# Kernel tuning notes

Hardware: AMD Instinct MI355X
Metric: run time of the kernel (lower is better)

The kernel has to match this reference:

```python
import jax, jax.numpy as jnp
import numpy as np

N, M, H, R, F = 50000, 64, 128, 4, 7   # nodes, latent, hidden, rounds, node features
E = 800_000                             # directed edges
B, NMAX = 32, 512                       # dense-batch graphs, padded nodes per graph


def setup_inputs() -> dict:
    key = jax.random.key(0)
    ks = jax.random.split(key, 10)
    glorot = lambda k, shape, fan_in: (jax.random.normal(k, shape, jnp.float32)
                                       / np.float32(np.sqrt(fan_in)))
    return {
        "z": jax.random.normal(ks[0], (N, M), jnp.float32),
        "edge_index": jax.random.randint(ks[1], (2, E), 0, N, dtype=jnp.int32),
        "z_dense": jax.random.normal(ks[2], (B, NMAX, M), jnp.float32),
        "bias": jnp.zeros((1,), jnp.float32),
        "W_in": glorot(ks[3], (M, H), M), "b_in": jnp.zeros((H,), jnp.float32),
        "W_msg": glorot(ks[4], (R, H, H), H), "b_msg": jnp.zeros((R, H), jnp.float32),
        "W_upd": glorot(ks[5], (R, H, H), H), "b_upd": jnp.zeros((R, H), jnp.float32),
        "W_out": glorot(ks[6], (H, F), H), "b_out": jnp.zeros((F,), jnp.float32),
    }


def reference(z, edge_index, z_dense, bias, W_in, b_in, W_msg, b_msg,
              W_upd, b_upd, W_out, b_out):
    # decode_edges: (B, n_max, M) -> (B, n_max, n_max) inner-product logits + bias
    edge_logits = jnp.einsum("bnm,bkm->bnk", z_dense, z_dense) + bias[0]

    # decode_nodes: gather -> MLP -> scatter message passing
    src, dst = edge_index[0], edge_index[1]
    num_nodes = z.shape[0]
    state = jax.nn.relu(z @ W_in + b_in)                      # (N, H)
    for r in range(W_msg.shape[0]):                           # R small, fixed
        message = jax.nn.relu(state @ W_msg[r] + b_msg[r])    # (N, H)
        # aggregated[v] = sum_{(u->v) in E} message[u]
        aggregated = jax.ops.segment_sum(message[src], dst, num_segments=num_nodes)
        state = state + jax.nn.relu(aggregated @ W_upd[r] + b_upd[r])
    node_logits = state @ W_out + b_out                       # (N, F)

    return edge_logits, node_logits
```

## Files before the change

kernel.cpp:

```cpp
#include <hip/hip_runtime.h>
#include <cstdint>

#define NN  50000
#define MD  64
#define HD  128
#define RR  4
#define FD  7
#define EE  800000
#define BG  32
#define NMX 512

#define NH   196
#define NBL  196
#define BE   4096
#define NS   (NH * NBL)
#define NSB  ((NS + 255) / 256)

typedef __attribute__((ext_vector_type(8))) short bf16x8;
typedef __attribute__((ext_vector_type(4))) float f32x4;

__device__ __forceinline__ unsigned short f2bf(float f) {
    unsigned u = __builtin_bit_cast(unsigned, f);
    u = (u + 0x7fffu + ((u >> 16) & 1u)) >> 16;
    return (unsigned short)u;
}
__device__ __forceinline__ float bflo(unsigned u) { return __builtin_bit_cast(float, u << 16); }
__device__ __forceinline__ float bfhi(unsigned u) { return __builtin_bit_cast(float, u & 0xffff0000u); }

__device__ __forceinline__ bf16x8 pack8(float4 a, float4 b) {
    bf16x8 r;
    r[0]=(short)f2bf(a.x); r[1]=(short)f2bf(a.y); r[2]=(short)f2bf(a.z); r[3]=(short)f2bf(a.w);
    r[4]=(short)f2bf(b.x); r[5]=(short)f2bf(b.y); r[6]=(short)f2bf(b.z); r[7]=(short)f2bf(b.w);
    return r;
}

__global__ __launch_bounds__(256) void edge_kernel(const unsigned short* __restrict__ zdb,
                                                   const float* __restrict__ bias,
                                                   float* __restrict__ out) {
    __shared__ float cstage[64][68];
    const int b  = blockIdx.z;
    const int tn = blockIdx.y * 64;
    const int tk = blockIdx.x * 64;
    const unsigned short* zb = zdb + (size_t)b * NMX * MD;
    const int tid = threadIdx.x, wave = tid >> 6, lane = tid & 63;
    const int l15 = lane & 15, k8 = (lane >> 4) * 8;

    const unsigned short* ap = zb + (size_t)(tn + wave * 16 + l15) * MD + k8;
    bf16x8 af0 = *(const bf16x8*)ap;
    bf16x8 af1 = *(const bf16x8*)(ap + 32);

    f32x4 acc[4];
    #pragma unroll
    for (int ct = 0; ct < 4; ct++) acc[ct] = (f32x4){0.f, 0.f, 0.f, 0.f};
    const unsigned short* bp = zb + (size_t)(tk + l15) * MD + k8;
    #pragma unroll
    for (int ct = 0; ct < 4; ct++) {
        bf16x8 b0 = *(const bf16x8*)(bp + (size_t)ct * 16 * MD);
        bf16x8 b1 = *(const bf16x8*)(bp + (size_t)ct * 16 * MD + 32);
        acc[ct] = __builtin_amdgcn_mfma_f32_16x16x32_bf16(af0, b0, acc[ct], 0, 0, 0);
        acc[ct] = __builtin_amdgcn_mfma_f32_16x16x32_bf16(af1, b1, acc[ct], 0, 0, 0);
    }
    #pragma unroll
    for (int ct = 0; ct < 4; ct++)
        #pragma unroll
        for (int i = 0; i < 4; i++)
            cstage[wave * 16 + (lane >> 4) * 4 + i][ct * 16 + l15] = acc[ct][i];
    __syncthreads();
    const float bi = bias[0];
    #pragma unroll
    for (int it = 0; it < 4; it++) {
        int f = tid + it * 256;
        int row = f >> 4, c4 = (f & 15) * 4;
        float4 v = *(const float4*)&cstage[row][c4];
        v.x += bi; v.y += bi; v.z += bi; v.w += bi;
        *(float4*)(out + ((size_t)b * NMX + tn + row) * NMX + tk + c4) = v;
    }
}

__global__ __launch_bounds__(256) void cvt_kernel(const float* __restrict__ src,
                                                  unsigned short* __restrict__ dst,
                                                  int n4) {
    int i = blockIdx.x * 256 + threadIdx.x;
    if (i >= n4) return;
    float4 v = *(const float4*)(src + (size_t)i * 4);
    ushort4 o = {f2bf(v.x), f2bf(v.y), f2bf(v.z), f2bf(v.w)};
    *(ushort4*)(dst + (size_t)i * 4) = o;
}

__global__ __launch_bounds__(256) void tcvt_kernel(const float* __restrict__ src,
                                                   unsigned short* __restrict__ dst,
                                                   int K, int H) {
    int r = blockIdx.y;
    int i = blockIdx.x * 256 + threadIdx.x;
    if (i >= K * H) return;
    int k = i / H, h = i % H;
    float v = src[(size_t)r * K * H + i];
    dst[(size_t)r * K * H + (size_t)h * K + k] = f2bf(v);
}

template <int K1, int MODE>
__global__ __launch_bounds__(256) void fused_kernel(
    const unsigned short* __restrict__ in,
    const unsigned short* __restrict__ Wt1,
    const float* __restrict__ b1,
    float* __restrict__ state,
    const unsigned short* __restrict__ Wt2,
    const float* __restrict__ b2,
    unsigned short* __restrict__ msgb,
    const float* __restrict__ Wout,
    const float* __restrict__ bout,
    float* __restrict__ node_out,
    int nrows)
{
    constexpr int KC1 = K1 / 32;
    __shared__ float cstage[64][132];
    __shared__ float sWout[MODE == 2 ? HD * FD : 1];
    const int tid = threadIdx.x, wave = tid >> 6, lane = tid & 63;
    const int l15 = lane & 15, k8 = (lane >> 4) * 8;
    const int rbase = blockIdx.x * 64;

    if constexpr (MODE == 2)
        for (int i = tid; i < HD * FD; i += 256) sWout[i] = Wout[i];

    int rclamp = min(rbase + wave * 16 + l15, nrows - 1);
    bf16x8 af[KC1];
    #pragma unroll
    for (int c = 0; c < KC1; c++)
        af[c] = *(const bf16x8*)(in + (size_t)rclamp * K1 + (size_t)c * 32 + k8);
    f32x4 acc[8];
    #pragma unroll
    for (int ct = 0; ct < 8; ct++) acc[ct] = (f32x4){0.f, 0.f, 0.f, 0.f};
    const unsigned short* bp = Wt1 + (size_t)l15 * K1 + k8;
    #pragma unroll
    for (int ct = 0; ct < 8; ct++)
        #pragma unroll
        for (int c = 0; c < KC1; c++) {
            bf16x8 bf = *(const bf16x8*)(bp + (size_t)ct * 16 * K1 + c * 32);
            acc[ct] = __builtin_amdgcn_mfma_f32_16x16x32_bf16(af[c], bf, acc[ct], 0, 0, 0);
        }
    #pragma unroll
    for (int ct = 0; ct < 8; ct++)
        #pragma unroll
        for (int i = 0; i < 4; i++)
            cstage[wave * 16 + (lane >> 4) * 4 + i][ct * 16 + l15] = acc[ct][i];
    __syncthreads();

    #pragma unroll
    for (int it = 0; it < 8; it++) {
        int f = tid + it * 256;
        int row = f >> 5, c4 = (f & 31) * 4;
        int grow = rbase + row;
        if (grow < nrows) {
            float4 v = *(const float4*)&cstage[row][c4];
            float4 bb = *(const float4*)(b1 + c4);
            v.x = fmaxf(v.x + bb.x, 0.f);
            v.y = fmaxf(v.y + bb.y, 0.f);
            v.z = fmaxf(v.z + bb.z, 0.f);
            v.w = fmaxf(v.w + bb.w, 0.f);
            if constexpr (MODE >= 1) {
                float4 so = *(const float4*)(state + (size_t)grow * HD + c4);
                v.x += so.x; v.y += so.y; v.z += so.z; v.w += so.w;
            }
            if constexpr (MODE <= 1)
                *(float4*)(state + (size_t)grow * HD + c4) = v;
            *(float4*)&cstage[row][c4] = v;
        }
    }
    __syncthreads();

    if constexpr (MODE <= 1) {
        bf16x8 af2[4];
        #pragma unroll
        for (int c = 0; c < 4; c++) {
            float4 u0 = *(const float4*)&cstage[wave * 16 + l15][c * 32 + k8];
            float4 u1 = *(const float4*)&cstage[wave * 16 + l15][c * 32 + k8 + 4];
            af2[c] = pack8(u0, u1);
        }
        f32x4 acc2[8];
        #pragma unroll
        for (int ct = 0; ct < 8; ct++) acc2[ct] = (f32x4){0.f, 0.f, 0.f, 0.f};
        const unsigned short* bp2 = Wt2 + (size_t)l15 * HD + k8;
        #pragma unroll
        for (int ct = 0; ct < 8; ct++)
            #pragma unroll
            for (int c = 0; c < 4; c++) {
                bf16x8 bf = *(const bf16x8*)(bp2 + (size_t)ct * 16 * HD + c * 32);
                acc2[ct] = __builtin_amdgcn_mfma_f32_16x16x32_bf16(af2[c], bf, acc2[ct], 0, 0, 0);
            }
        __syncthreads();
        #pragma unroll
        for (int ct = 0; ct < 8; ct++)
            #pragma unroll
            for (int i = 0; i < 4; i++)
                cstage[wave * 16 + (lane >> 4) * 4 + i][ct * 16 + l15] = acc2[ct][i];
        __syncthreads();
        #pragma unroll
        for (int it = 0; it < 8; it++) {
            int f = tid + it * 256;
            int row = f >> 5, c4 = (f & 31) * 4;
            int grow = rbase + row;
            if (grow < nrows) {
                float4 v = *(const float4*)&cstage[row][c4];
                float4 bb = *(const float4*)(b2 + c4);
                v.x = fmaxf(v.x + bb.x, 0.f);
                v.y = fmaxf(v.y + bb.y, 0.f);
                v.z = fmaxf(v.z + bb.z, 0.f);
                v.w = fmaxf(v.w + bb.w, 0.f);
                ushort4 o = {f2bf(v.x), f2bf(v.y), f2bf(v.z), f2bf(v.w)};
                *(ushort4*)(msgb + (size_t)grow * HD + c4) = o;
            }
        }
    } else {
        for (int i = tid; i < 64 * FD; i += 256) {
            int row = i / FD, ff = i - row * FD;
            int grow = rbase + row;
            if (grow < nrows) {
                float a = bout[ff];
                #pragma unroll 8
                for (int k = 0; k < HD; k++)
                    a += cstage[row][k] * sWout[k * FD + ff];
                node_out[(size_t)grow * FD + ff] = a;
            }
        }
    }
}

__global__ __launch_bounds__(256) void p1c_kernel(const int* __restrict__ dst,
                                                  int* __restrict__ bh) {
    __shared__ int h[NH];
    const int b = blockIdx.x;
    for (int i = threadIdx.x; i < NH; i += 256) h[i] = 0;
    __syncthreads();
    const int e0 = b * BE;
    for (int i = threadIdx.x; i < BE; i += 256) {
        int e = e0 + i;
        if (e < EE) atomicAdd(&h[dst[e] >> 8], 1);
    }
    __syncthreads();
    for (int i = threadIdx.x; i < NH; i += 256) bh[i * NBL + b] = h[i];
}

__global__ __launch_bounds__(256) void scan1_kernel(const int* __restrict__ in,
                                                    int* __restrict__ incl,
                                                    int* __restrict__ bsum, int n) {
    __shared__ int s[256];
    int i = blockIdx.x * 256 + threadIdx.x;
    int t = threadIdx.x;
    s[t] = (i < n) ? in[i] : 0;
    __syncthreads();
    #pragma unroll
    for (int off = 1; off < 256; off <<= 1) {
        int x = (t >= off) ? s[t - off] : 0;
        __syncthreads();
        s[t] += x;
        __syncthreads();
    }
    if (i < n) incl[i] = s[t];
    if (t == 255) bsum[blockIdx.x] = s[255];
}

__global__ __launch_bounds__(256) void scan2_kernel(int* __restrict__ bsum, int nb) {
    __shared__ int s[256];
    int t = threadIdx.x;
    int orig = (t < nb) ? bsum[t] : 0;
    s[t] = orig;
    __syncthreads();
    #pragma unroll
    for (int off = 1; off < 256; off <<= 1) {
        int x = (t >= off) ? s[t - off] : 0;
        __syncthreads();
        s[t] += x;
        __syncthreads();
    }
    if (t < nb) bsum[t] = s[t] - orig;
}

__global__ __launch_bounds__(256) void scanex_kernel(const int* __restrict__ in,
                                                     const int* __restrict__ incl,
                                                     const int* __restrict__ bsum,
                                                     int* __restrict__ ex, int n) {
    int i = blockIdx.x * 256 + threadIdx.x;
    if (i < n) ex[i] = incl[i] - in[i] + bsum[blockIdx.x];
}

__global__ __launch_bounds__(256) void p1s_kernel(const int* __restrict__ src,
                                                  const int* __restrict__ dst,
                                                  const int* __restrict__ ex,
                                                  int2* __restrict__ sorted) {
    __shared__ int cur[NH];
    const int b = blockIdx.x;
    for (int i = threadIdx.x; i < NH; i += 256) cur[i] = ex[i * NBL + b];
    __syncthreads();
    const int e0 = b * BE;
    for (int i = threadIdx.x; i < BE; i += 256) {
        int e = e0 + i;
        if (e < EE) {
            int d = dst[e];
            int pos = atomicAdd(&cur[d >> 8], 1);
            sorted[pos] = make_int2(d, src[e]);
        }
    }
}

__global__ __launch_bounds__(256) void p2_kernel(const int2* __restrict__ sorted,
                                                 const int* __restrict__ ex,
                                                 int* __restrict__ row_ptr,
                                                 int* __restrict__ colsrc) {
    __shared__ int hist[256];
    __shared__ int scanb[256];
    __shared__ int cur[256];
    const int h = blockIdx.x;
    const int t = threadIdx.x;
    const int base = ex[h * NBL];
    const int endp = (h == NH - 1) ? EE : ex[(h + 1) * NBL];
    const int cnt  = endp - base;
    hist[t] = 0;
    __syncthreads();
    for (int i = t; i < cnt; i += 256)
        atomicAdd(&hist[sorted[base + i].x & 255], 1);
    __syncthreads();
    scanb[t] = hist[t];
    __syncthreads();
    #pragma unroll
    for (int off = 1; off < 256; off <<= 1) {
        int x = (t >= off) ? scanb[t - off] : 0;
        __syncthreads();
        scanb[t] += x;
        __syncthreads();
    }
    int excl = scanb[t] - hist[t];
    cur[t] = excl;
    int v = h * 256 + t;
    if (v < NN) row_ptr[v] = base + excl;
    if (h == NH - 1 && t == 0) row_ptr[NN] = EE;
    __syncthreads();
    for (int i = t; i < cnt; i += 256) {
        int2 pr = sorted[base + i];
        int pos = base + atomicAdd(&cur[pr.x & 255], 1);
        colsrc[pos] = pr.y;
    }
}

__global__ __launch_bounds__(256) void gather_kernel(const int* __restrict__ rp,
                                                     const int* __restrict__ colsrc,
                                                     const uint4* __restrict__ msg4,
                                                     uint4* __restrict__ agg4) {
    int v = blockIdx.x * 4 + (threadIdx.x >> 6);
    if (v >= NN) return;
    const int lane = threadIdx.x & 63;
    const int e = lane >> 4, q = lane & 15;
    const int beg = rp[v], end = rp[v + 1];
    float a[8];
    #pragma unroll
    for (int i = 0; i < 8; i++) a[i] = 0.f;

    int j = beg;
    for (; j + 7 < end; j += 8) {
        int c0 = colsrc[j + e];
        int c1 = colsrc[j + 4 + e];
        uint4 u = msg4[(size_t)c0 * 16 + q];
        uint4 w = msg4[(size_t)c1 * 16 + q];
        a[0] += bflo(u.x); a[1] += bfhi(u.x);
        a[2] += bflo(u.y); a[3] += bfhi(u.y);
        a[4] += bflo(u.z); a[5] += bfhi(u.z);
        a[6] += bflo(u.w); a[7] += bfhi(u.w);
        a[0] += bflo(w.x); a[1] += bfhi(w.x);
        a[2] += bflo(w.y); a[3] += bfhi(w.y);
        a[4] += bflo(w.z); a[5] += bfhi(w.z);
        a[6] += bflo(w.w); a[7] += bfhi(w.w);
    }
    for (; j < end; j += 4) {
        if (j + e < end) {
            uint4 u = msg4[(size_t)colsrc[j + e] * 16 + q];
            a[0] += bflo(u.x); a[1] += bfhi(u.x);
            a[2] += bflo(u.y); a[3] += bfhi(u.y);
            a[4] += bflo(u.z); a[5] += bfhi(u.z);
            a[6] += bflo(u.w); a[7] += bfhi(u.w);
        }
    }
    #pragma unroll
    for (int i = 0; i < 8; i++) {
        a[i] += __shfl_xor(a[i], 16);
        a[i] += __shfl_xor(a[i], 32);
    }
    if (lane < 16) {
        uint4 o;
        o.x = (unsigned)f2bf(a[0]) | ((unsigned)f2bf(a[1]) << 16);
        o.y = (unsigned)f2bf(a[2]) | ((unsigned)f2bf(a[3]) << 16);
        o.z = (unsigned)f2bf(a[4]) | ((unsigned)f2bf(a[5]) << 16);
        o.w = (unsigned)f2bf(a[6]) | ((unsigned)f2bf(a[7]) << 16);
        agg4[(size_t)v * 16 + q] = o;
    }
}

extern "C" void kernel_launch(void* const* d_in, const int* in_sizes, int n_in,
                              void* d_out, int out_size, void* d_ws, size_t ws_size,
                              hipStream_t stream) {
    const float* z          = (const float*)d_in[0];
    const int*   edge_index = (const int*)  d_in[1];
    const float* z_dense    = (const float*)d_in[2];
    const float* bias       = (const float*)d_in[3];
    const float* W_in       = (const float*)d_in[4];
    const float* b_in       = (const float*)d_in[5];
    const float* W_msg      = (const float*)d_in[6];
    const float* b_msg      = (const float*)d_in[7];
    const float* W_upd      = (const float*)d_in[8];
    const float* b_upd      = (const float*)d_in[9];
    const float* W_out      = (const float*)d_in[10];
    const float* b_out      = (const float*)d_in[11];

    float* out      = (float*)d_out;
    float* edge_out = out;
    float* node_out = out + (size_t)BG * NMX * NMX;

    char* p = (char*)d_ws;
    float* state = (float*)p;                     p += (size_t)NN * HD * 4;
    unsigned short* msgb   = (unsigned short*)p;  p += (size_t)NN * HD * 2;
    unsigned short* aggb   = (unsigned short*)p;  p += (size_t)NN * HD * 2;
    unsigned short* zb     = (unsigned short*)p;  p += (size_t)NN * MD * 2;
    unsigned short* zdb    = (unsigned short*)p;  p += (size_t)BG * NMX * MD * 2;
    unsigned short* wt_in  = (unsigned short*)p;  p += (size_t)HD * MD * 2;
    unsigned short* wt_msg = (unsigned short*)p;  p += (size_t)RR * HD * HD * 2;
    unsigned short* wt_upd = (unsigned short*)p;  p += (size_t)RR * HD * HD * 2;
    int*  bh      = (int*)p;                      p += (size_t)NS * 4;
    int*  incl    = (int*)p;                      p += (size_t)NS * 4;
    int*  exsc    = (int*)p;                      p += (size_t)NS * 4;
    int*  row_ptr = (int*)p;                      p += (size_t)(NN + 1) * 4;
    int*  colsrc  = (int*)p;                      p += (size_t)EE * 4;
    int2* sorted  = (int2*)p;                     p += (size_t)EE * 8;
    int*  bsum    = (int*)p;

    const int* src = edge_index;
    const int* dst = edge_index + EE;

    cvt_kernel<<<(BG * NMX * MD / 4 + 255) / 256, 256, 0, stream>>>(
        z_dense, zdb, BG * NMX * MD / 4);
    dim3 eg(NMX / 64, NMX / 64, BG);
    edge_kernel<<<eg, 256, 0, stream>>>(zdb, bias, edge_out);

    cvt_kernel<<<(NN * MD / 4 + 255) / 256, 256, 0, stream>>>(z, zb, NN * MD / 4);
    tcvt_kernel<<<dim3((MD * HD + 255) / 256, 1), 256, 0, stream>>>(W_in, wt_in, MD, HD);
    tcvt_kernel<<<dim3((HD * HD + 255) / 256, RR), 256, 0, stream>>>(W_msg, wt_msg, HD, HD);
    tcvt_kernel<<<dim3((HD * HD + 255) / 256, RR), 256, 0, stream>>>(W_upd, wt_upd, HD, HD);

    p1c_kernel<<<NBL, 256, 0, stream>>>(dst, bh);
    scan1_kernel<<<NSB, 256, 0, stream>>>(bh, incl, bsum, NS);
    scan2_kernel<<<1, 256, 0, stream>>>(bsum, NSB);
    scanex_kernel<<<NSB, 256, 0, stream>>>(bh, incl, bsum, exsc, NS);
    p1s_kernel<<<NBL, 256, 0, stream>>>(src, dst, exsc, sorted);
    p2_kernel<<<NH, 256, 0, stream>>>(sorted, exsc, row_ptr, colsrc);

    const int MG = (NN + 63) / 64;
    const int GG = (NN + 3) / 4;

    fused_kernel<MD, 0><<<MG, 256, 0, stream>>>(
        zb, wt_in, b_in, state,
        wt_msg, b_msg, msgb, nullptr, nullptr, nullptr, NN);

    for (int r = 0; r < RR - 1; r++) {
        gather_kernel<<<GG, 256, 0, stream>>>(row_ptr, colsrc,
                                              (const uint4*)msgb, (uint4*)aggb);
        fused_kernel<HD, 1><<<MG, 256, 0, stream>>>(
            aggb, wt_upd + (size_t)r * HD * HD, b_upd + (size_t)r * HD, state,
            wt_msg + (size_t)(r + 1) * HD * HD, b_msg + (size_t)(r + 1) * HD,
            msgb, nullptr, nullptr, nullptr, NN);
    }
    gather_kernel<<<GG, 256, 0, stream>>>(row_ptr, colsrc,
                                          (const uint4*)msgb, (uint4*)aggb);
    fused_kernel<HD, 2><<<MG, 256, 0, stream>>>(
        aggb, wt_upd + (size_t)(RR - 1) * HD * HD, b_upd + (size_t)(RR - 1) * HD, state,
        nullptr, nullptr, nullptr, W_out, b_out, node_out, NN);
}
```

Measured before the change: 359.6 us.

## Split message features into column blocks and gather in four passes

Message and aggregate buffers move from row-major [N,128] to four column blocks of [N,32] bf16. The gather kernel runs one pass per block, so each pass reads from a 3.2 MB slice that fits in cache better than the full 12.8 MB table. Each wave now covers 16 edges at once with 4 lanes per edge and reduces with extra shuffles. Edge-index loads and aggregate stores become nontemporal. The cost is reading colsrc four times and doing more shuffle work per node.

```diff
diff --git a/kernel.cpp b/kernel.cpp
--- a/kernel.cpp
+++ b/kernel.cpp
@@ -16,8 +16,12 @@
 #define NS   (NH * NBL)
 #define NSB  ((NS + 255) / 256)
 
+#define NPASS 4
+#define GNBP  ((NN + 3) / 4)
+
 typedef __attribute__((ext_vector_type(8))) short bf16x8;
 typedef __attribute__((ext_vector_type(4))) float f32x4;
+typedef __attribute__((ext_vector_type(4))) unsigned u32x4;
 
 __device__ __forceinline__ unsigned short f2bf(float f) {
     unsigned u = __builtin_bit_cast(unsigned, f);
@@ -98,7 +102,7 @@
     dst[(size_t)r * K * H + (size_t)h * K + k] = f2bf(v);
 }
 
-template <int K1, int MODE>
+template <int K1, int MODE, bool BLK>
 __global__ __launch_bounds__(256) void fused_kernel(
     const unsigned short* __restrict__ in,
     const unsigned short* __restrict__ Wt1,
@@ -125,8 +129,11 @@
     int rclamp = min(rbase + wave * 16 + l15, nrows - 1);
     bf16x8 af[KC1];
     #pragma unroll
-    for (int c = 0; c < KC1; c++)
-        af[c] = *(const bf16x8*)(in + (size_t)rclamp * K1 + (size_t)c * 32 + k8);
+    for (int c = 0; c < KC1; c++) {
+        size_t off = BLK ? ((size_t)c * NN * 32 + (size_t)rclamp * 32 + k8)
+                         : ((size_t)rclamp * K1 + (size_t)c * 32 + k8);
+        af[c] = *(const bf16x8*)(in + off);
+    }
     f32x4 acc[8];
     #pragma unroll
     for (int ct = 0; ct < 8; ct++) acc[ct] = (f32x4){0.f, 0.f, 0.f, 0.f};
@@ -207,7 +214,8 @@
                 v.z = fmaxf(v.z + bb.z, 0.f);
                 v.w = fmaxf(v.w + bb.w, 0.f);
                 ushort4 o = {f2bf(v.x), f2bf(v.y), f2bf(v.z), f2bf(v.w)};
-                *(ushort4*)(msgb + (size_t)grow * HD + c4) = o;
+                size_t off = (size_t)(c4 >> 5) * NN * 32 + (size_t)grow * 32 + (c4 & 31);
+                *(ushort4*)(msgb + off) = o;
             }
         }
     } else {
@@ -343,23 +351,27 @@
 
 __global__ __launch_bounds__(256) void gather_kernel(const int* __restrict__ rp,
                                                      const int* __restrict__ colsrc,
-                                                     const uint4* __restrict__ msg4,
-                                                     uint4* __restrict__ agg4) {
-    int v = blockIdx.x * 4 + (threadIdx.x >> 6);
+                                                     const u32x4* __restrict__ msg4,
+                                                     u32x4* __restrict__ agg4) {
+    const int pass = blockIdx.x / GNBP;
+    const int nb   = blockIdx.x - pass * GNBP;
+    const int v    = nb * 4 + (threadIdx.x >> 6);
     if (v >= NN) return;
     const int lane = threadIdx.x & 63;
-    const int e = lane >> 4, q = lane & 15;
+    const int e = lane >> 2, q = lane & 3;
     const int beg = rp[v], end = rp[v + 1];
+    const u32x4* mbase = msg4 + (size_t)pass * NN * 4 + q;
+
     float a[8];
     #pragma unroll
     for (int i = 0; i < 8; i++) a[i] = 0.f;
 
     int j = beg;
-    for (; j + 7 < end; j += 8) {
-        int c0 = colsrc[j + e];
-        int c1 = colsrc[j + 4 + e];
-        uint4 u = msg4[(size_t)c0 * 16 + q];
-        uint4 w = msg4[(size_t)c1 * 16 + q];
+    for (; j + 31 < end; j += 32) {
+        int c0 = __builtin_nontemporal_load(&colsrc[j + e]);
+        int c1 = __builtin_nontemporal_load(&colsrc[j + 16 + e]);
+        u32x4 u = mbase[(size_t)c0 * 4];
+        u32x4 w = mbase[(size_t)c1 * 4];
         a[0] += bflo(u.x); a[1] += bfhi(u.x);
         a[2] += bflo(u.y); a[3] += bfhi(u.y);
         a[4] += bflo(u.z); a[5] += bfhi(u.z);
@@ -369,9 +381,10 @@
         a[4] += bflo(w.z); a[5] += bfhi(w.z);
         a[6] += bflo(w.w); a[7] += bfhi(w.w);
     }
-    for (; j < end; j += 4) {
+    for (; j < end; j += 16) {
         if (j + e < end) {
-            uint4 u = msg4[(size_t)colsrc[j + e] * 16 + q];
+            int c0 = __builtin_nontemporal_load(&colsrc[j + e]);
+            u32x4 u = mbase[(size_t)c0 * 4];
             a[0] += bflo(u.x); a[1] += bfhi(u.x);
             a[2] += bflo(u.y); a[3] += bfhi(u.y);
             a[4] += bflo(u.z); a[5] += bfhi(u.z);
@@ -380,16 +393,18 @@
     }
     #pragma unroll
     for (int i = 0; i < 8; i++) {
+        a[i] += __shfl_xor(a[i], 4);
+        a[i] += __shfl_xor(a[i], 8);
         a[i] += __shfl_xor(a[i], 16);
         a[i] += __shfl_xor(a[i], 32);
     }
-    if (lane < 16) {
-        uint4 o;
+    if (lane < 4) {
+        u32x4 o;
         o.x = (unsigned)f2bf(a[0]) | ((unsigned)f2bf(a[1]) << 16);
         o.y = (unsigned)f2bf(a[2]) | ((unsigned)f2bf(a[3]) << 16);
         o.z = (unsigned)f2bf(a[4]) | ((unsigned)f2bf(a[5]) << 16);
         o.w = (unsigned)f2bf(a[6]) | ((unsigned)f2bf(a[7]) << 16);
-        agg4[(size_t)v * 16 + q] = o;
+        __builtin_nontemporal_store(o, &agg4[(size_t)pass * NN * 4 + (size_t)v * 4 + lane]);
     }
 }
 
@@ -451,23 +466,23 @@
     p2_kernel<<<NH, 256, 0, stream>>>(sorted, exsc, row_ptr, colsrc);
 
     const int MG = (NN + 63) / 64;
-    const int GG = (NN + 3) / 4;
-
-    fused_kernel<MD, 0><<<MG, 256, 0, stream>>>(
+    const int GG = NPASS * GNBP;
+
+    fused_kernel<MD, 0, false><<<MG, 256, 0, stream>>>(
         zb, wt_in, b_in, state,
         wt_msg, b_msg, msgb, nullptr, nullptr, nullptr, NN);
 
     for (int r = 0; r < RR - 1; r++) {
         gather_kernel<<<GG, 256, 0, stream>>>(row_ptr, colsrc,
-                                              (const uint4*)msgb, (uint4*)aggb);
-        fused_kernel<HD, 1><<<MG, 256, 0, stream>>>(
+                                              (const u32x4*)msgb, (u32x4*)aggb);
+        fused_kernel<HD, 1, true><<<MG, 256, 0, stream>>>(
             aggb, wt_upd + (size_t)r * HD * HD, b_upd + (size_t)r * HD, state,
             wt_msg + (size_t)(r + 1) * HD * HD, b_msg + (size_t)(r + 1) * HD,
             msgb, nullptr, nullptr, nullptr, NN);
     }
     gather_kernel<<<GG, 256, 0, stream>>>(row_ptr, colsrc,
-                                          (const uint4*)msgb, (uint4*)aggb);
-    fused_kernel<HD, 2><<<MG, 256, 0, stream>>>(
+                                          (const u32x4*)msgb, (u32x4*)aggb);
+    fused_kernel<HD, 2, true><<<MG, 256, 0, stream>>>(
         aggb, wt_upd + (size_t)(RR - 1) * HD * HD, b_upd + (size_t)(RR - 1) * HD, state,
         nullptr, nullptr, nullptr, W_out, b_out, node_out, NN);
 }
```

Result: slower. 538.4 us (+49.7%).

## Fuse neighbor gather into per-round GEMM kernel and merge conversion launches

Applied to the files above, without the earlier changes.

The separate gather kernel is removed. Each fused GEMM block now aggregates neighbor messages for its 64 rows into shared memory before the MFMA step, with message buffers ping-ponged between rounds. This avoids writing and re-reading the aggregated bf16 buffer and cuts kernel launches. The conversion kernels are also merged into fewer launches. In exchange, each wave processes 16 nodes serially in the gather, which lowers memory-level parallelism compared to one wave per node.

```diff
diff --git a/kernel.cpp b/kernel.cpp
--- a/kernel.cpp
+++ b/kernel.cpp
@@ -18,6 +18,7 @@
 
 typedef __attribute__((ext_vector_type(8))) short bf16x8;
 typedef __attribute__((ext_vector_type(4))) float f32x4;
+typedef __attribute__((ext_vector_type(4))) unsigned u32x4;
 
 __device__ __forceinline__ unsigned short f2bf(float f) {
     unsigned u = __builtin_bit_cast(unsigned, f);
@@ -77,30 +78,46 @@
     }
 }
 
-__global__ __launch_bounds__(256) void cvt_kernel(const float* __restrict__ src,
-                                                  unsigned short* __restrict__ dst,
-                                                  int n4) {
+__global__ __launch_bounds__(256) void cvt2_kernel(const float* __restrict__ a,
+                                                   unsigned short* __restrict__ da, int n4a,
+                                                   const float* __restrict__ b,
+                                                   unsigned short* __restrict__ db, int n4b) {
     int i = blockIdx.x * 256 + threadIdx.x;
-    if (i >= n4) return;
-    float4 v = *(const float4*)(src + (size_t)i * 4);
-    ushort4 o = {f2bf(v.x), f2bf(v.y), f2bf(v.z), f2bf(v.w)};
-    *(ushort4*)(dst + (size_t)i * 4) = o;
-}
-
-__global__ __launch_bounds__(256) void tcvt_kernel(const float* __restrict__ src,
-                                                   unsigned short* __restrict__ dst,
-                                                   int K, int H) {
-    int r = blockIdx.y;
+    if (i < n4a) {
+        float4 v = *(const float4*)(a + (size_t)i * 4);
+        ushort4 o = {f2bf(v.x), f2bf(v.y), f2bf(v.z), f2bf(v.w)};
+        *(ushort4*)(da + (size_t)i * 4) = o;
+    } else if (i < n4a + n4b) {
+        int k = i - n4a;
+        float4 v = *(const float4*)(b + (size_t)k * 4);
+        ushort4 o = {f2bf(v.x), f2bf(v.y), f2bf(v.z), f2bf(v.w)};
+        *(ushort4*)(db + (size_t)k * 4) = o;
+    }
+}
+
+__global__ __launch_bounds__(256) void tcvt_all_kernel(const float* __restrict__ W_in,
+                                                       const float* __restrict__ W_msg,
+                                                       const float* __restrict__ W_upd,
+                                                       unsigned short* __restrict__ wt_in,
+                                                       unsigned short* __restrict__ wt_msg,
+                                                       unsigned short* __restrict__ wt_upd) {
+    const int y = blockIdx.y;
+    const float* src; unsigned short* dst; int K;
+    if (y == 0)        { src = W_in;                      dst = wt_in;                       K = MD; }
+    else if (y <= RR)  { int r = y - 1;     src = W_msg + (size_t)r * HD * HD; dst = wt_msg + (size_t)r * HD * HD; K = HD; }
+    else               { int r = y - 1 - RR; src = W_upd + (size_t)r * HD * HD; dst = wt_upd + (size_t)r * HD * HD; K = HD; }
     int i = blockIdx.x * 256 + threadIdx.x;
-    if (i >= K * H) return;
-    int k = i / H, h = i % H;
-    float v = src[(size_t)r * K * H + i];
-    dst[(size_t)r * K * H + (size_t)h * K + k] = f2bf(v);
-}
-
-template <int K1, int MODE>
+    if (i >= K * HD) return;
+    int k = i / HD, h = i % HD;
+    dst[(size_t)h * K + k] = f2bf(src[i]);
+}
+
+template <int K1, int MODE, bool GATH>
 __global__ __launch_bounds__(256) void fused_kernel(
     const unsigned short* __restrict__ in,
+    const int* __restrict__ rp,
+    const int* __restrict__ colsrc,
+    const u32x4* __restrict__ msg4,
     const unsigned short* __restrict__ Wt1,
     const float* __restrict__ b1,
     float* __restrict__ state,
@@ -114,6 +131,7 @@
 {
     constexpr int KC1 = K1 / 32;
     __shared__ float cstage[64][132];
+    __shared__ unsigned short atile[GATH ? 64 : 1][GATH ? 136 : 8];
     __shared__ float sWout[MODE == 2 ? HD * FD : 1];
     const int tid = threadIdx.x, wave = tid >> 6, lane = tid & 63;
     const int l15 = lane & 15, k8 = (lane >> 4) * 8;
@@ -122,11 +140,65 @@
     if constexpr (MODE == 2)
         for (int i = tid; i < HD * FD; i += 256) sWout[i] = Wout[i];
 
-    int rclamp = min(rbase + wave * 16 + l15, nrows - 1);
+    if constexpr (GATH) {
+        const int e = lane >> 4, q = lane & 15;
+        for (int t = 0; t < 16; t++) {
+            const int v = rbase + wave * 16 + t;
+            float a[8];
+            #pragma unroll
+            for (int i = 0; i < 8; i++) a[i] = 0.f;
+            if (v < nrows) {
+                const int beg = rp[v], end = rp[v + 1];
+                int j = beg;
+                for (; j + 7 < end; j += 8) {
+                    int c0 = colsrc[j + e];
+                    int c1 = colsrc[j + 4 + e];
+                    u32x4 u = msg4[(size_t)c0 * 16 + q];
+                    u32x4 w = msg4[(size_t)c1 * 16 + q];
+                    a[0] += bflo(u.x); a[1] += bfhi(u.x);
+                    a[2] += bflo(u.y); a[3] += bfhi(u.y);
+                    a[4] += bflo(u.z); a[5] += bfhi(u.z);
+                    a[6] += bflo(u.w); a[7] += bfhi(u.w);
+                    a[0] += bflo(w.x); a[1] += bfhi(w.x);
+                    a[2] += bflo(w.y); a[3] += bfhi(w.y);
+                    a[4] += bflo(w.z); a[5] += bfhi(w.z);
+                    a[6] += bflo(w.w); a[7] += bfhi(w.w);
+                }
+                for (; j < end; j += 4) {
+                    if (j + e < end) {
+                        u32x4 u = msg4[(size_t)colsrc[j + e] * 16 + q];
+                        a[0] += bflo(u.x); a[1] += bfhi(u.x);
+                        a[2] += bflo(u.y); a[3] += bfhi(u.y);
+                        a[4] += bflo(u.z); a[5] += bfhi(u.z);
+                        a[6] += bflo(u.w); a[7] += bfhi(u.w);
+                    }
+                }
+                #pragma unroll
+                for (int i = 0; i < 8; i++) {
+                    a[i] += __shfl_xor(a[i], 16);
+                    a[i] += __shfl_xor(a[i], 32);
+                }
+            }
+            if (lane < 16) {
+                bf16x8 o;
+                #pragma unroll
+                for (int i = 0; i < 8; i++) o[i] = (short)f2bf(a[i]);
+                *(bf16x8*)&atile[wave * 16 + t][lane * 8] = o;
+            }
+        }
+    }
+
     bf16x8 af[KC1];
-    #pragma unroll
-    for (int c = 0; c < KC1; c++)
-        af[c] = *(const bf16x8*)(in + (size_t)rclamp * K1 + (size_t)c * 32 + k8);
+    if constexpr (GATH) {
+        #pragma unroll
+        for (int c = 0; c < KC1; c++)
+            af[c] = *(const bf16x8*)&atile[wave * 16 + l15][c * 32 + k8];
+    } else {
+        int rclamp = min(rbase + wave * 16 + l15, nrows - 1);
+        #pragma unroll
+        for (int c = 0; c < KC1; c++)
+            af[c] = *(const bf16x8*)(in + (size_t)rclamp * K1 + (size_t)c * 32 + k8);
+    }
     f32x4 acc[8];
     #pragma unroll
     for (int ct = 0; ct < 8; ct++) acc[ct] = (f32x4){0.f, 0.f, 0.f, 0.f};
@@ -338,58 +410,6 @@
         int2 pr = sorted[base + i];
         int pos = base + atomicAdd(&cur[pr.x & 255], 1);
         colsrc[pos] = pr.y;
-    }
-}
-
-__global__ __launch_bounds__(256) void gather_kernel(const int* __restrict__ rp,
-                                                     const int* __restrict__ colsrc,
-                                                     const uint4* __restrict__ msg4,
-                                                     uint4* __restrict__ agg4) {
-    int v = blockIdx.x * 4 + (threadIdx.x >> 6);
-    if (v >= NN) return;
-    const int lane = threadIdx.x & 63;
-    const int e = lane >> 4, q = lane & 15;
-    const int beg = rp[v], end = rp[v + 1];
-    float a[8];
-    #pragma unroll
-    for (int i = 0; i < 8; i++) a[i] = 0.f;
-
-    int j = beg;
-    for (; j + 7 < end; j += 8) {
-        int c0 = colsrc[j + e];
-        int c1 = colsrc[j + 4 + e];
-        uint4 u = msg4[(size_t)c0 * 16 + q];
-        uint4 w = msg4[(size_t)c1 * 16 + q];
-        a[0] += bflo(u.x); a[1] += bfhi(u.x);
-        a[2] += bflo(u.y); a[3] += bfhi(u.y);
-        a[4] += bflo(u.z); a[5] += bfhi(u.z);
-        a[6] += bflo(u.w); a[7] += bfhi(u.w);
-        a[0] += bflo(w.x); a[1] += bfhi(w.x);
-        a[2] += bflo(w.y); a[3] += bfhi(w.y);
-        a[4] += bflo(w.z); a[5] += bfhi(w.z);
-        a[6] += bflo(w.w); a[7] += bfhi(w.w);
-    }
-    for (; j < end; j += 4) {
-        if (j + e < end) {
-            uint4 u = msg4[(size_t)colsrc[j + e] * 16 + q];
-            a[0] += bflo(u.x); a[1] += bfhi(u.x);
-            a[2] += bflo(u.y); a[3] += bfhi(u.y);
-            a[4] += bflo(u.z); a[5] += bfhi(u.z);
-            a[6] += bflo(u.w); a[7] += bfhi(u.w);
-        }
-    }
-    #pragma unroll
-    for (int i = 0; i < 8; i++) {
-        a[i] += __shfl_xor(a[i], 16);
-        a[i] += __shfl_xor(a[i], 32);
-    }
-    if (lane < 16) {
-        uint4 o;
-        o.x = (unsigned)f2bf(a[0]) | ((unsigned)f2bf(a[1]) << 16);
-        o.y = (unsigned)f2bf(a[2]) | ((unsigned)f2bf(a[3]) << 16);
-        o.z = (unsigned)f2bf(a[4]) | ((unsigned)f2bf(a[5]) << 16);
-        o.w = (unsigned)f2bf(a[6]) | ((unsigned)f2bf(a[7]) << 16);
-        agg4[(size_t)v * 16 + q] = o;
     }
 }
 
@@ -415,8 +435,8 @@
 
     char* p = (char*)d_ws;
     float* state = (float*)p;                     p += (size_t)NN * HD * 4;
-    unsigned short* msgb   = (unsigned short*)p;  p += (size_t)NN * HD * 2;
-    unsigned short* aggb   = (unsigned short*)p;  p += (size_t)NN * HD * 2;
+    unsigned short* msgA   = (unsigned short*)p;  p += (size_t)NN * HD * 2;
+    unsigned short* msgB   = (unsigned short*)p;  p += (size_t)NN * HD * 2;
     unsigned short* zb     = (unsigned short*)p;  p += (size_t)NN * MD * 2;
     unsigned short* zdb    = (unsigned short*)p;  p += (size_t)BG * NMX * MD * 2;
     unsigned short* wt_in  = (unsigned short*)p;  p += (size_t)HD * MD * 2;
@@ -433,15 +453,16 @@
     const int* src = edge_index;
     const int* dst = edge_index + EE;
 
-    cvt_kernel<<<(BG * NMX * MD / 4 + 255) / 256, 256, 0, stream>>>(
-        z_dense, zdb, BG * NMX * MD / 4);
+    const int n4zd = BG * NMX * MD / 4;
+    const int n4z  = NN * MD / 4;
+    cvt2_kernel<<<(n4zd + n4z + 255) / 256, 256, 0, stream>>>(
+        z_dense, zdb, n4zd, z, zb, n4z);
+
     dim3 eg(NMX / 64, NMX / 64, BG);
     edge_kernel<<<eg, 256, 0, stream>>>(zdb, bias, edge_out);
 
-    cvt_kernel<<<(NN * MD / 4 + 255) / 256, 256, 0, stream>>>(z, zb, NN * MD / 4);
-    tcvt_kernel<<<dim3((MD * HD + 255) / 256, 1), 256, 0, stream>>>(W_in, wt_in, MD, HD);
-    tcvt_kernel<<<dim3((HD * HD + 255) / 256, RR), 256, 0, stream>>>(W_msg, wt_msg, HD, HD);
-    tcvt_kernel<<<dim3((HD * HD + 255) / 256, RR), 256, 0, stream>>>(W_upd, wt_upd, HD, HD);
+    tcvt_all_kernel<<<dim3((HD * HD + 255) / 256, 1 + 2 * RR), 256, 0, stream>>>(
+        W_in, W_msg, W_upd, wt_in, wt_msg, wt_upd);
 
     p1c_kernel<<<NBL, 256, 0, stream>>>(dst, bh);
     scan1_kernel<<<NSB, 256, 0, stream>>>(bh, incl, bsum, NS);
@@ -451,23 +472,23 @@
     p2_kernel<<<NH, 256, 0, stream>>>(sorted, exsc, row_ptr, colsrc);
 
     const int MG = (NN + 63) / 64;
-    const int GG = (NN + 3) / 4;
-
-    fused_kernel<MD, 0><<<MG, 256, 0, stream>>>(
-        zb, wt_in, b_in, state,
-        wt_msg, b_msg, msgb, nullptr, nullptr, nullptr, NN);
-
+
+    fused_kernel<MD, 0, false><<<MG, 256, 0, stream>>>(
+        zb, nullptr, nullptr, nullptr, wt_in, b_in, state,
+        wt_msg, b_msg, msgA, nullptr, nullptr, nullptr, NN);
+
+    unsigned short* ping = msgA;
+    unsigned short* pong = msgB;
     for (int r = 0; r < RR - 1; r++) {
-        gather_kernel<<<GG, 256, 0, stream>>>(row_ptr, colsrc,
-                                              (const uint4*)msgb, (uint4*)aggb);
-        fused_kernel<HD, 1><<<MG, 256, 0, stream>>>(
-            aggb, wt_upd + (size_t)r * HD * HD, b_upd + (size_t)r * HD, state,
+        fused_kernel<HD, 1, true><<<MG, 256, 0, stream>>>(
+            nullptr, row_ptr, colsrc, (const u32x4*)ping,
+            wt_upd + (size_t)r * HD * HD, b_upd + (size_t)r * HD, state,
             wt_msg + (size_t)(r + 1) * HD * HD, b_msg + (size_t)(r + 1) * HD,
-            msgb, nullptr, nullptr, nullptr, NN);
-    }
-    gather_kernel<<<GG, 256, 0, stream>>>(row_ptr, colsrc,
-                                          (const uint4*)msgb, (uint4*)aggb);
-    fused_kernel<HD, 2><<<MG, 256, 0, stream>>>(
-        aggb, wt_upd + (size_t)(RR - 1) * HD * HD, b_upd + (size_t)(RR - 1) * HD, state,
+            pong, nullptr, nullptr, nullptr, NN);
+        unsigned short* tmp = ping; ping = pong; pong = tmp;
+    }
+    fused_kernel<HD, 2, true><<<MG, 256, 0, stream>>>(
+        nullptr, row_ptr, colsrc, (const u32x4*)ping,
+        wt_upd + (size_t)(RR - 1) * HD * HD, b_upd + (size_t)(RR - 1) * HD, state,
         nullptr, nullptr, nullptr, W_out, b_out, node_out, NN);
 }
```

Result: slower. 526.1 us (+46.3%).
